# Optimization experiments

Hardware: AMD Instinct MI355X
Metric: run time of the kernel (lower is better)

## Reference

```python
import jax, jax.numpy as jnp
import numpy as np

D_MODEL = 1024
N_HEADS = 16
D_K = D_MODEL // N_HEADS  # 64
THETA = 10000.0


def _rope(x, token_positions):
    # x: [b, h, s, d], token_positions: [s]
    inv_freq = 1.0 / THETA ** (jnp.arange(0, D_K, 2, dtype=jnp.float32) / D_K)  # [d/2]
    ang = token_positions.astype(jnp.float32)[:, None] * inv_freq               # [s, d/2]
    cos, sin = jnp.cos(ang), jnp.sin(ang)                                       # broadcast over b,h
    x1 = x[..., 0::2]
    x2 = x[..., 1::2]
    even = x1 * cos - x2 * sin
    odd = x1 * sin + x2 * cos
    return jnp.stack([even, odd], axis=-1).reshape(x.shape)  # re-interleave


def setup_inputs() -> dict:
    key = jax.random.key(0)
    k1, k2, k3 = jax.random.split(key, 3)
    B, S = 2, 2048
    x = jax.random.normal(k1, (B, S, D_MODEL), dtype=jnp.float32)
    token_positions = jnp.arange(S, dtype=jnp.int32)
    std_qkv = np.sqrt(2.0 / (D_MODEL + 3 * D_MODEL))
    std_out = np.sqrt(2.0 / (D_MODEL + D_MODEL))
    W_qkv = jax.random.normal(k2, (3 * D_MODEL, D_MODEL), dtype=jnp.float32) * std_qkv
    W_out = jax.random.normal(k3, (D_MODEL, D_MODEL), dtype=jnp.float32) * std_out
    return {"x": x, "token_positions": token_positions, "W_qkv": W_qkv, "W_out": W_out}


def reference(x, token_positions, W_qkv, W_out):
    B, S, _ = x.shape
    qkv = jnp.einsum('bsi,oi->bso', x, W_qkv)                 # [b, s, 3*h*d]
    qkv = qkv.reshape(B, S, 3, N_HEADS, D_K)
    qkv = jnp.transpose(qkv, (2, 0, 3, 1, 4))                 # [3, b, h, s, d]
    q, k, v = qkv[0], qkv[1], qkv[2]
    q = _rope(q, token_positions)
    k = _rope(k, token_positions)
    scores = jnp.einsum('bhqd,bhkd->bhqk', q, k) / jnp.sqrt(jnp.float32(D_K))
    mask = jnp.tril(jnp.ones((S, S), dtype=bool))
    scores = jnp.where(mask, scores, -jnp.inf)
    attn = jax.nn.softmax(scores, axis=-1)
    out = jnp.einsum('bhqk,bhkd->bhqd', attn, v)              # [b, h, s, d]
    out = jnp.transpose(out, (0, 2, 1, 3)).reshape(B, S, D_MODEL)
    return jnp.einsum('bsi,oi->bso', out, W_out)
```

## Files before the change

### kernel.cpp

```cpp
#include <hip/hip_runtime.h>
#include <hip/hip_bf16.h>
#include <math.h>

#define D_MODEL 1024
#define N_HEADS 16
#define D_K     64
#define S_LEN   2048
#define B_SZ    2

typedef unsigned short u16;
typedef unsigned int   u32;
using short8 = __attribute__((ext_vector_type(8))) short;
using f32x4  = __attribute__((ext_vector_type(4))) float;

__device__ inline float bf2f(u16 u) { return __uint_as_float((u32)u << 16); }
__device__ inline u16 f2bf(float f) {
    __hip_bfloat16 h = __float2bfloat16(f);
    return *(u16*)&h;
}
__device__ inline void gload_lds16(const void* g, void* l) {
    __builtin_amdgcn_global_load_lds(
        (const __attribute__((address_space(1))) unsigned int*)g,
        (__attribute__((address_space(3))) unsigned int*)l, 16, 0, 0);
}

__global__ __launch_bounds__(256)
void cast3_f32_bf16(const float* __restrict__ a, u16* __restrict__ ao, int na4,
                    const float* __restrict__ bsrc, u16* __restrict__ bo, int nb4,
                    const float* __restrict__ c, u16* __restrict__ co, int nc4) {
    int j = blockIdx.x * 256 + threadIdx.x;
    const float* src; u16* dst;
    if (j < na4) { src = a; dst = ao; }
    else {
        j -= na4;
        if (j < nb4) { src = bsrc; dst = bo; }
        else {
            j -= nb4;
            if (j >= nc4) return;
            src = c; dst = co;
        }
    }
    float4 v = ((const float4*)src)[j];
    ushort4 u;
    u.x = f2bf(v.x); u.y = f2bf(v.y); u.z = f2bf(v.z); u.w = f2bf(v.w);
    ((ushort4*)dst)[j] = u;
}

template <bool OUT_BF16>
__global__ __launch_bounds__(256)
void gemm_bt_mfma(const u16* __restrict__ A, const u16* __restrict__ B,
                  void* __restrict__ Cout, int M, int N, int K) {
    __shared__ u16 As[128 * 32];
    __shared__ u16 Bs[128 * 32];
    const int tid  = threadIdx.x;
    const int lane = tid & 63;
    const int wv   = tid >> 6;
    const int wm   = wv >> 1, wn = wv & 1;
    const int row0 = blockIdx.y * 128;
    const int col0 = blockIdx.x * 128;

    const int lr = lane >> 2;
    const int lc = (lane & 3) * 8;

    f32x4 acc[4][4] = {};

    for (int k0 = 0; k0 < K; k0 += 32) {
#pragma unroll
        for (int t = 0; t < 2; t++) {
            int rblk = wv * 32 + t * 16;
            gload_lds16(A + (size_t)(row0 + rblk + lr) * K + k0 + lc, &As[rblk * 32]);
            gload_lds16(B + (size_t)(col0 + rblk + lr) * K + k0 + lc, &Bs[rblk * 32]);
        }
        __syncthreads();

        short8 af[4], bfr[4];
#pragma unroll
        for (int mi = 0; mi < 4; mi++)
            af[mi] = *(const short8*)&As[(wm * 64 + mi * 16 + (lane & 15)) * 32 + (lane >> 4) * 8];
#pragma unroll
        for (int nj = 0; nj < 4; nj++)
            bfr[nj] = *(const short8*)&Bs[(wn * 64 + nj * 16 + (lane & 15)) * 32 + (lane >> 4) * 8];
#pragma unroll
        for (int mi = 0; mi < 4; mi++)
#pragma unroll
            for (int nj = 0; nj < 4; nj++)
                acc[mi][nj] = __builtin_amdgcn_mfma_f32_16x16x32_bf16(
                    af[mi], bfr[nj], acc[mi][nj], 0, 0, 0);
        __syncthreads();
    }

    const int cr = (lane >> 4) * 4;
    const int cc = lane & 15;
#pragma unroll
    for (int mi = 0; mi < 4; mi++) {
#pragma unroll
        for (int nj = 0; nj < 4; nj++) {
            int c = col0 + wn * 64 + nj * 16 + cc;
#pragma unroll
            for (int r = 0; r < 4; r++) {
                int rr = row0 + wm * 64 + mi * 16 + cr + r;
                if (OUT_BF16)
                    ((u16*)Cout)[(size_t)rr * N + c] = f2bf(acc[mi][nj][r]);
                else
                    ((float*)Cout)[(size_t)rr * N + c] = acc[mi][nj][r];
            }
        }
    }
}

__global__ __launch_bounds__(256)
void rope_bf16(u16* __restrict__ qkv, const int* __restrict__ pos) {
    int idx = blockIdx.x * blockDim.x + threadIdx.x;
    int j = idx & 31;
    int h = (idx >> 5) & 15;
    int w = (idx >> 9) & 1;
    int s = (idx >> 10) & 2047;
    int b = idx >> 21;

    float p = (float)pos[s];
    float inv_freq = __powf(10000.0f, -(float)(2 * j) / 64.0f);
    float ang = p * inv_freq;
    float sn, cs;
    sincosf(ang, &sn, &cs);
    float sc = (w == 0) ? 0.125f : 1.0f;

    size_t base = (((size_t)(b * S_LEN + s) * 3 + w) * D_MODEL) + h * D_K + 2 * j;
    float x1 = bf2f(qkv[base]);
    float x2 = bf2f(qkv[base + 1]);
    qkv[base]     = f2bf((x1 * cs - x2 * sn) * sc);
    qkv[base + 1] = f2bf((x1 * sn + x2 * cs) * sc);
}

__global__ __launch_bounds__(256)
void vtrans(const u16* __restrict__ qkv, u16* __restrict__ VT) {
    __shared__ u16 t[64][68];
    const int st = blockIdx.x, h = blockIdx.y, b = blockIdx.z;
    const int tid = threadIdx.x;
    const int bh = b * N_HEADS + h;

#pragma unroll
    for (int i = 0; i < 4; i++) {
        int e  = tid + i * 256;
        int sl = e >> 4;
        int c4 = e & 15;
        ushort4 v = *(const ushort4*)&qkv[((size_t)(b * S_LEN + st * 64 + sl) * 3 + 2) * D_MODEL
                                          + h * D_K + c4 * 4];
        *(ushort4*)&t[sl][c4 * 4] = v;
    }
    __syncthreads();
#pragma unroll
    for (int i = 0; i < 4; i++) {
        int e  = tid + i * 256;
        int d  = e >> 4;
        int s4 = e & 15;
        ushort4 o;
        o.x = t[s4 * 4 + 0][d];
        o.y = t[s4 * 4 + 1][d];
        o.z = t[s4 * 4 + 2][d];
        o.w = t[s4 * 4 + 3][d];
        *(ushort4*)&VT[((size_t)bh * D_K + d) * S_LEN + st * 64 + s4 * 4] = o;
    }
}

__device__ __forceinline__ void attn_step(
    const u16* __restrict__ Ksc, const u16* __restrict__ Vsc,
    u16* __restrict__ Psw,
    short8 (&qf)[2], f32x4 (&acc)[4], float& mq, float& lq,
    int k0, int qw0, bool diag, int l15, int quad)
{
    f32x4 s[4] = {};
    __builtin_amdgcn_s_setprio(1);
#pragma unroll
    for (int kf = 0; kf < 2; kf++)
#pragma unroll
        for (int nj = 0; nj < 4; nj++) {
            short8 kfr = *(const short8*)&Ksc[kf * 2048 + (nj * 16 + l15) * 32 + quad * 8];
            s[nj] = __builtin_amdgcn_mfma_f32_16x16x32_bf16(kfr, qf[kf], s[nj], 0, 0, 0);
        }
    __builtin_amdgcn_s_setprio(0);

    if (diag) {
        const int row_g = qw0 + l15;
#pragma unroll
        for (int nj = 0; nj < 4; nj++)
#pragma unroll
            for (int r = 0; r < 4; r++) {
                int key_g = k0 + nj * 16 + quad * 4 + r;
                if (key_g > row_g) s[nj][r] = -INFINITY;
            }
    }

    float rmax = s[0][0];
#pragma unroll
    for (int nj = 0; nj < 4; nj++)
#pragma unroll
        for (int r = 0; r < 4; r++) rmax = fmaxf(rmax, s[nj][r]);
    rmax = fmaxf(rmax, __shfl_xor(rmax, 16, 64));
    rmax = fmaxf(rmax, __shfl_xor(rmax, 32, 64));

    if (!__all(rmax <= mq + 8.f)) {
        float mn = fmaxf(mq, rmax);
        float alpha = __expf(mq - mn);
        mq = mn;
        lq *= alpha;
#pragma unroll
        for (int nj = 0; nj < 4; nj++)
#pragma unroll
            for (int r = 0; r < 4; r++) acc[nj][r] *= alpha;
    }

    float rsum = 0.f;
#pragma unroll
    for (int nj = 0; nj < 4; nj++)
#pragma unroll
        for (int r = 0; r < 4; r++) {
            float p = __expf(s[nj][r] - mq);
            s[nj][r] = p;
            rsum += p;
        }
    rsum += __shfl_xor(rsum, 16, 64);
    rsum += __shfl_xor(rsum, 32, 64);
    lq += rsum;

#pragma unroll
    for (int nj = 0; nj < 4; nj++) {
        u32 lo = ((u32)f2bf(s[nj][1]) << 16) | f2bf(s[nj][0]);
        u32 hi = ((u32)f2bf(s[nj][3]) << 16) | f2bf(s[nj][2]);
        uint2 pk; pk.x = lo; pk.y = hi;
        *(uint2*)&Psw[l15 * 68 + nj * 16 + quad * 4] = pk;
    }

    __builtin_amdgcn_s_setprio(1);
#pragma unroll
    for (int kf = 0; kf < 2; kf++) {
        const u16* pp = &Psw[l15 * 68 + kf * 32 + quad * 8];
        uint2 plo = *(const uint2*)pp;
        uint2 phi = *(const uint2*)(pp + 4);
        u32 praw[4] = { plo.x, plo.y, phi.x, phi.y };
        short8 pf = *(const short8*)praw;
#pragma unroll
        for (int nj = 0; nj < 4; nj++) {
            short8 vf = *(const short8*)&Vsc[kf * 2048 + (nj * 16 + l15) * 32 + quad * 8];
            acc[nj] = __builtin_amdgcn_mfma_f32_16x16x32_bf16(vf, pf, acc[nj], 0, 0, 0);
        }
    }
    __builtin_amdgcn_s_setprio(0);
}

__global__ __launch_bounds__(256)
void attn_mfma(const u16* __restrict__ qkv, const u16* __restrict__ VT,
               u16* __restrict__ out, float* __restrict__ partO,
               float* __restrict__ partML) {
    __shared__ u16 Ks[2][64 * 32];
    __shared__ u16 VsT[2][64 * 32];
    __shared__ u16 Ps[4][16 * 68];

    const int tid  = threadIdx.x;
    const int lane = tid & 63;
    const int wv   = tid >> 6;

    const int bid  = blockIdx.x;
    const int idx  = bid >> 3;
    const int bh   = (bid & 7) * 4 + (idx >> 5);
    const int rem  = idx & 31;
    const int pr   = rem >> 1;
    const int role = rem & 1;
    const int qtH  = 31 - pr;
    const int qtL  = pr;
    const int h    = bh & (N_HEADS - 1);
    const int b    = bh >> 4;

    const int l15  = lane & 15;
    const int quad = lane >> 4;
    const int qw0H = qtH * 64 + wv * 16;

    const size_t vtb = (size_t)bh * D_K * S_LEN;
    u16* Psw = &Ps[wv][0];
    const int lr = lane >> 2;
    const int lc = (lane & 3) * 8;

    auto STAGE = [&](int kts) {
        const int k0s = kts * 64;
#pragma unroll
        for (int kf = 0; kf < 2; kf++)
            gload_lds16(qkv + ((size_t)(b * S_LEN + k0s + wv * 16 + lr) * 3 + 1) * D_MODEL
                            + h * D_K + kf * 32 + lc,
                        &Ks[kf][(wv * 16) * 32]);
#pragma unroll
        for (int kc = 0; kc < 2; kc++)
            gload_lds16(VT + vtb + (size_t)(wv * 16 + lr) * S_LEN + k0s + kc * 32 + lc,
                        &VsT[kc][(wv * 16) * 32]);
    };

    short8 qfH[2];
#pragma unroll
    for (int kf = 0; kf < 2; kf++)
        qfH[kf] = *(const short8*)&qkv[((size_t)(b * S_LEN + qw0H + l15) * 3 + 0) * D_MODEL
                                       + h * D_K + kf * 32 + quad * 8];
    f32x4 accH[4] = {};
    float mqH = -INFINITY, lqH = 0.f;

    const int kbeg = role ? 17 : 0;
    const int kend = role ? qtH : 16;
    for (int kt = kbeg; kt <= kend; kt++) {
        STAGE(kt);
        __syncthreads();
        attn_step(&Ks[0][0], &VsT[0][0], Psw, qfH, accH, mqH, lqH,
                  kt * 64, qw0H, kt == qtH, l15, quad);
        __syncthreads();
    }

    {
        const size_t unit = (size_t)(bh * 16 + (qtH - 16)) * 2 + role;
        float* Od = partO + unit * 4096 + (size_t)(wv * 16 + l15) * 64;
#pragma unroll
        for (int nj = 0; nj < 4; nj++)
            *(f32x4*)&Od[nj * 16 + quad * 4] = accH[nj];
        if (quad == 0) {
            float* ML = partML + unit * 128;
            ML[wv * 16 + l15]      = mqH;
            ML[64 + wv * 16 + l15] = lqH;
        }
    }

    if (!role) return;

    const int qw0L = qtL * 64 + wv * 16;
    short8 qfL[2];
#pragma unroll
    for (int kf = 0; kf < 2; kf++)
        qfL[kf] = *(const short8*)&qkv[((size_t)(b * S_LEN + qw0L + l15) * 3 + 0) * D_MODEL
                                       + h * D_K + kf * 32 + quad * 8];
    f32x4 accL[4] = {};
    float mqL = -INFINITY, lqL = 0.f;

    for (int kt = 0; kt <= qtL; kt++) {
        STAGE(kt);
        __syncthreads();
        attn_step(&Ks[0][0], &VsT[0][0], Psw, qfL, accL, mqL, lqL,
                  kt * 64, qw0L, kt == qtL, l15, quad);
        __syncthreads();
    }

    float invl = 1.f / lqL;
#pragma unroll
    for (int nj = 0; nj < 4; nj++) {
        ushort4 o;
        o.x = f2bf(accL[nj][0] * invl); o.y = f2bf(accL[nj][1] * invl);
        o.z = f2bf(accL[nj][2] * invl); o.w = f2bf(accL[nj][3] * invl);
        *(ushort4*)&out[(size_t)(b * S_LEN + qw0L + l15) * D_MODEL
                        + h * D_K + nj * 16 + quad * 4] = o;
    }
}

__global__ __launch_bounds__(256)
void attn_combine(const float* __restrict__ partO, const float* __restrict__ partML,
                  u16* __restrict__ out) {
    const int t16 = blockIdx.x & 15;
    const int bh  = blockIdx.x >> 4;
    const int h = bh & (N_HEADS - 1), b = bh >> 4;
    const int q0 = (t16 + 16) * 64;
    const int tid = threadIdx.x;
    const int q  = tid >> 2;
    const int d0 = (tid & 3) * 16;

    const size_t u0 = (size_t)(bh * 16 + t16) * 2;
    const float* O0 = partO + u0 * 4096;
    const float* O1 = O0 + 4096;
    const float* ML0 = partML + u0 * 128;
    const float* ML1 = ML0 + 128;

    float m0 = ML0[q], l0 = ML0[64 + q];
    float m1 = ML1[q], l1 = ML1[64 + q];
    float ms = fmaxf(m0, m1);
    float f0 = __expf(m0 - ms), f1 = __expf(m1 - ms);
    float inv = 1.f / (l0 * f0 + l1 * f1);
    f0 *= inv; f1 *= inv;
#pragma unroll
    for (int i = 0; i < 4; i++) {
        float4 a = *(const float4*)&O0[q * 64 + d0 + i * 4];
        float4 c = *(const float4*)&O1[q * 64 + d0 + i * 4];
        ushort4 o;
        o.x = f2bf(a.x * f0 + c.x * f1);
        o.y = f2bf(a.y * f0 + c.y * f1);
        o.z = f2bf(a.z * f0 + c.z * f1);
        o.w = f2bf(a.w * f0 + c.w * f1);
        *(ushort4*)&out[(size_t)(b * S_LEN + q0 + q) * D_MODEL + h * D_K + d0 + i * 4] = o;
    }
}

extern "C" void kernel_launch(void* const* d_in, const int* in_sizes, int n_in,
                              void* d_out, int out_size, void* d_ws, size_t ws_size,
                              hipStream_t stream) {
    const float* x    = (const float*)d_in[0];
    const int*   pos  = (const int*)d_in[1];
    const float* Wqkv = (const float*)d_in[2];
    const float* Wout = (const float*)d_in[3];
    float*       out  = (float*)d_out;

    const int M = B_SZ * S_LEN;

    u16* qkvb = (u16*)d_ws;
    u16* aob  = qkvb + (size_t)M * 3 * D_MODEL;
    u16* xb   = aob  + (size_t)M * D_MODEL;
    u16* wqb  = xb   + (size_t)M * D_MODEL;
    u16* wob  = wqb  + (size_t)3 * D_MODEL * D_MODEL;
    u16* vtb  = wob  + (size_t)D_MODEL * D_MODEL;
    float* partO  = (float*)(vtb + (size_t)M * D_MODEL);
    float* partML = partO + (size_t)1024 * 4096;

    const int na4 = M * D_MODEL / 4;
    const int nb4 = 3 * D_MODEL * D_MODEL / 4;
    const int nc4 = D_MODEL * D_MODEL / 4;
    cast3_f32_bf16<<<(na4 + nb4 + nc4 + 255) / 256, 256, 0, stream>>>(
        x, xb, na4, Wqkv, wqb, nb4, Wout, wob, nc4);

    gemm_bt_mfma<true><<<dim3(3 * D_MODEL / 128, M / 128), 256, 0, stream>>>(
        xb, wqb, qkvb, M, 3 * D_MODEL, D_MODEL);

    rope_bf16<<<(B_SZ * S_LEN * 2 * N_HEADS * 32) / 256, 256, 0, stream>>>(qkvb, pos);

    vtrans<<<dim3(S_LEN / 64, N_HEADS, B_SZ), 256, 0, stream>>>(qkvb, vtb);

    attn_mfma<<<1024, 256, 0, stream>>>(qkvb, vtb, aob, partO, partML);
    attn_combine<<<512, 256, 0, stream>>>(partO, partML, aob);

    gemm_bt_mfma<false><<<dim3(D_MODEL / 128, M / 128), 256, 0, stream>>>(
        aob, wob, out, M, D_MODEL, D_MODEL);
}
```

Measured before the change: 216.2 us.

## Fuse RoPE and V-transpose kernels, vectorize RoPE, swizzle attention LDS tiles

Merges the separate RoPE and V-transpose launches into one kernel whose blocks split by index, which removes one kernel launch. The RoPE part now handles 8 bf16 values per thread with a 16-byte load and store and uses exp2f and fast __sincosf instead of powf and sincosf. Separately, the attention kernel applies an XOR swizzle to the K and V^T LDS staging layout and the matching fragment reads, meant to cut LDS bank conflicts. The fast sincos loses accuracy at large angles (positions up to 2047), which could affect numerical tolerance.

```diff
diff --git a/kernel.cpp b/kernel.cpp
--- a/kernel.cpp
+++ b/kernel.cpp
@@ -10,8 +10,9 @@
 
 typedef unsigned short u16;
 typedef unsigned int   u32;
-using short8 = __attribute__((ext_vector_type(8))) short;
-using f32x4  = __attribute__((ext_vector_type(4))) float;
+using short8  = __attribute__((ext_vector_type(8))) short;
+using ushort8 = __attribute__((ext_vector_type(8))) unsigned short;
+using f32x4   = __attribute__((ext_vector_type(4))) float;
 
 __device__ inline float bf2f(u16 u) { return __uint_as_float((u32)u << 16); }
 __device__ inline u16 f2bf(float f) {
@@ -109,64 +110,73 @@
 }
 
 __global__ __launch_bounds__(256)
-void rope_bf16(u16* __restrict__ qkv, const int* __restrict__ pos) {
-    int idx = blockIdx.x * blockDim.x + threadIdx.x;
-    int j = idx & 31;
-    int h = (idx >> 5) & 15;
-    int w = (idx >> 9) & 1;
-    int s = (idx >> 10) & 2047;
-    int b = idx >> 21;
-
-    float p = (float)pos[s];
-    float inv_freq = __powf(10000.0f, -(float)(2 * j) / 64.0f);
-    float ang = p * inv_freq;
-    float sn, cs;
-    sincosf(ang, &sn, &cs);
+void prep_vtrans_rope(u16* __restrict__ qkv, u16* __restrict__ VT,
+                      const int* __restrict__ pos) {
+    const int bid = blockIdx.x;
+    const int tid = threadIdx.x;
+
+    if (bid < 1024) {
+        __shared__ u16 t[64][68];
+        const int st = bid & 31, h = (bid >> 5) & 15, b = bid >> 9;
+        const int bh = b * N_HEADS + h;
+#pragma unroll
+        for (int i = 0; i < 4; i++) {
+            int e  = tid + i * 256;
+            int sl = e >> 4;
+            int c4 = e & 15;
+            ushort4 v = *(const ushort4*)&qkv[((size_t)(b * S_LEN + st * 64 + sl) * 3 + 2) * D_MODEL
+                                              + h * D_K + c4 * 4];
+            *(ushort4*)&t[sl][c4 * 4] = v;
+        }
+        __syncthreads();
+#pragma unroll
+        for (int i = 0; i < 4; i++) {
+            int e  = tid + i * 256;
+            int d  = e >> 4;
+            int s4 = e & 15;
+            ushort4 o;
+            o.x = t[s4 * 4 + 0][d];
+            o.y = t[s4 * 4 + 1][d];
+            o.z = t[s4 * 4 + 2][d];
+            o.w = t[s4 * 4 + 3][d];
+            *(ushort4*)&VT[((size_t)bh * D_K + d) * S_LEN + st * 64 + s4 * 4] = o;
+        }
+        return;
+    }
+
+    int e  = (bid - 1024) * 256 + tid;
+    int j8 = e & 7;
+    int h  = (e >> 3) & 15;
+    int w  = (e >> 7) & 1;
+    int s  = (e >> 8) & 2047;
+    int b  = e >> 19;
+
+    float p  = (float)pos[s];
     float sc = (w == 0) ? 0.125f : 1.0f;
 
-    size_t base = (((size_t)(b * S_LEN + s) * 3 + w) * D_MODEL) + h * D_K + 2 * j;
-    float x1 = bf2f(qkv[base]);
-    float x2 = bf2f(qkv[base + 1]);
-    qkv[base]     = f2bf((x1 * cs - x2 * sn) * sc);
-    qkv[base + 1] = f2bf((x1 * sn + x2 * cs) * sc);
-}
-
-__global__ __launch_bounds__(256)
-void vtrans(const u16* __restrict__ qkv, u16* __restrict__ VT) {
-    __shared__ u16 t[64][68];
-    const int st = blockIdx.x, h = blockIdx.y, b = blockIdx.z;
-    const int tid = threadIdx.x;
-    const int bh = b * N_HEADS + h;
-
-#pragma unroll
-    for (int i = 0; i < 4; i++) {
-        int e  = tid + i * 256;
-        int sl = e >> 4;
-        int c4 = e & 15;
-        ushort4 v = *(const ushort4*)&qkv[((size_t)(b * S_LEN + st * 64 + sl) * 3 + 2) * D_MODEL
-                                          + h * D_K + c4 * 4];
-        *(ushort4*)&t[sl][c4 * 4] = v;
-    }
-    __syncthreads();
-#pragma unroll
-    for (int i = 0; i < 4; i++) {
-        int e  = tid + i * 256;
-        int d  = e >> 4;
-        int s4 = e & 15;
-        ushort4 o;
-        o.x = t[s4 * 4 + 0][d];
-        o.y = t[s4 * 4 + 1][d];
-        o.z = t[s4 * 4 + 2][d];
-        o.w = t[s4 * 4 + 3][d];
-        *(ushort4*)&VT[((size_t)bh * D_K + d) * S_LEN + st * 64 + s4 * 4] = o;
-    }
+    size_t base = (((size_t)(b * S_LEN + s) * 3 + w) * D_MODEL) + h * D_K + j8 * 8;
+    ushort8 v = *(const ushort8*)&qkv[base];
+
+    const float C = -0.41524101186092056f;
+#pragma unroll
+    for (int jj = 0; jj < 4; jj++) {
+        int j = j8 * 4 + jj;
+        float ang = p * exp2f((float)j * C);
+        float sn, cs;
+        __sincosf(ang, &sn, &cs);
+        float x1 = bf2f(v[2 * jj]);
+        float x2 = bf2f(v[2 * jj + 1]);
+        v[2 * jj]     = f2bf((x1 * cs - x2 * sn) * sc);
+        v[2 * jj + 1] = f2bf((x1 * sn + x2 * cs) * sc);
+    }
+    *(ushort8*)&qkv[base] = v;
 }
 
 __device__ __forceinline__ void attn_step(
     const u16* __restrict__ Ksc, const u16* __restrict__ Vsc,
     u16* __restrict__ Psw,
     short8 (&qf)[2], f32x4 (&acc)[4], float& mq, float& lq,
-    int k0, int qw0, bool diag, int l15, int quad)
+    int k0, int qw0, bool diag, int l15, int quad, int qsw)
 {
     f32x4 s[4] = {};
     __builtin_amdgcn_s_setprio(1);
@@ -174,7 +184,7 @@
     for (int kf = 0; kf < 2; kf++)
 #pragma unroll
         for (int nj = 0; nj < 4; nj++) {
-            short8 kfr = *(const short8*)&Ksc[kf * 2048 + (nj * 16 + l15) * 32 + quad * 8];
+            short8 kfr = *(const short8*)&Ksc[kf * 2048 + (nj * 16 + l15) * 32 + qsw * 8];
             s[nj] = __builtin_amdgcn_mfma_f32_16x16x32_bf16(kfr, qf[kf], s[nj], 0, 0, 0);
         }
     __builtin_amdgcn_s_setprio(0);
@@ -240,7 +250,7 @@
         short8 pf = *(const short8*)praw;
 #pragma unroll
         for (int nj = 0; nj < 4; nj++) {
-            short8 vf = *(const short8*)&Vsc[kf * 2048 + (nj * 16 + l15) * 32 + quad * 8];
+            short8 vf = *(const short8*)&Vsc[kf * 2048 + (nj * 16 + l15) * 32 + qsw * 8];
             acc[nj] = __builtin_amdgcn_mfma_f32_16x16x32_bf16(vf, pf, acc[nj], 0, 0, 0);
         }
     }
@@ -272,23 +282,24 @@
 
     const int l15  = lane & 15;
     const int quad = lane >> 4;
+    const int qsw  = quad ^ ((l15 >> 1) & 3);
     const int qw0H = qtH * 64 + wv * 16;
 
     const size_t vtb = (size_t)bh * D_K * S_LEN;
     u16* Psw = &Ps[wv][0];
-    const int lr = lane >> 2;
-    const int lc = (lane & 3) * 8;
+    const int lr  = lane >> 2;
+    const int csw = ((lane & 3) ^ ((lane >> 3) & 3)) * 8;
 
     auto STAGE = [&](int kts) {
         const int k0s = kts * 64;
 #pragma unroll
         for (int kf = 0; kf < 2; kf++)
             gload_lds16(qkv + ((size_t)(b * S_LEN + k0s + wv * 16 + lr) * 3 + 1) * D_MODEL
-                            + h * D_K + kf * 32 + lc,
+                            + h * D_K + kf * 32 + csw,
                         &Ks[kf][(wv * 16) * 32]);
 #pragma unroll
         for (int kc = 0; kc < 2; kc++)
-            gload_lds16(VT + vtb + (size_t)(wv * 16 + lr) * S_LEN + k0s + kc * 32 + lc,
+            gload_lds16(VT + vtb + (size_t)(wv * 16 + lr) * S_LEN + k0s + kc * 32 + csw,
                         &VsT[kc][(wv * 16) * 32]);
     };
 
@@ -306,7 +317,7 @@
         STAGE(kt);
         __syncthreads();
         attn_step(&Ks[0][0], &VsT[0][0], Psw, qfH, accH, mqH, lqH,
-                  kt * 64, qw0H, kt == qtH, l15, quad);
+                  kt * 64, qw0H, kt == qtH, l15, quad, qsw);
         __syncthreads();
     }
 
@@ -338,7 +349,7 @@
         STAGE(kt);
         __syncthreads();
         attn_step(&Ks[0][0], &VsT[0][0], Psw, qfL, accL, mqL, lqL,
-                  kt * 64, qw0L, kt == qtL, l15, quad);
+                  kt * 64, qw0L, kt == qtL, l15, quad, qsw);
         __syncthreads();
     }
 
@@ -418,9 +429,7 @@
     gemm_bt_mfma<true><<<dim3(3 * D_MODEL / 128, M / 128), 256, 0, stream>>>(
         xb, wqb, qkvb, M, 3 * D_MODEL, D_MODEL);
 
-    rope_bf16<<<(B_SZ * S_LEN * 2 * N_HEADS * 32) / 256, 256, 0, stream>>>(qkvb, pos);
-
-    vtrans<<<dim3(S_LEN / 64, N_HEADS, B_SZ), 256, 0, stream>>>(qkvb, vtb);
+    prep_vtrans_rope<<<5120, 256, 0, stream>>>(qkvb, vtb, pos);
 
     attn_mfma<<<1024, 256, 0, stream>>>(qkvb, vtb, aob, partO, partML);
     attn_combine<<<512, 256, 0, stream>>>(partO, partML, aob);
```

Result: faster. 197.6 us (-8.6%).
